# Optimization experiments

Measured on AMD Instinct MI355X. Metric: run time of the kernel, lower is better.

The kernel has to match this reference:

```python
import math
import jax, jax.numpy as jnp
import numpy as np

B, L, S, H, E, D = 2, 2048, 2048, 8, 64, 64


def setup_inputs() -> dict:
    key = jax.random.key(0)
    kq, kk, kv = jax.random.split(key, 3)
    return {
        "queries": jax.random.normal(kq, (B, L, H, E), dtype=jnp.float32),
        "keys": jax.random.normal(kk, (B, S, H, E), dtype=jnp.float32),
        "values": jax.random.normal(kv, (B, S, H, D), dtype=jnp.float32),
    }


def reference(queries, keys, values):
    b, l, h, e = queries.shape
    s = keys.shape[1]
    # source truncates queries if L > S
    if l > s:
        queries = queries[:, :s]
        l = s
    # dense scores [B,H,L,S]
    scores = jnp.einsum('blhe,bshe->bhls', queries, keys)
    # sparsity measure per query: max - mean over keys
    M_sp = scores.max(axis=-1) - scores.sum(axis=-1) / s  # [B,H,L]
    # k = min(max(L*log(S),1), L); for S>=3 this equals L (all queries, reordered)
    k = min(int(max(l * math.log(s), 1)), l)
    _, top_k = jax.lax.top_k(M_sp, k)  # [B,H,k], descending by M_sp
    # gather selected query rows of the score matrix
    topk_scores = jnp.take_along_axis(scores, top_k[..., None], axis=2)  # [B,H,k,S]
    topk_scores = topk_scores - topk_scores.max(axis=-1, keepdims=True)
    A = jax.nn.softmax(topk_scores / math.sqrt(e), axis=-1)  # [B,H,k,S]
    # attend (output in top-k-permuted query order, as in source)
    V = jnp.einsum('bhls,bshd->blhd', A, values)  # [B,k,H,D]
    return V
```

## Files before the change

kernel.cpp:

```cpp
#include <hip/hip_runtime.h>
#include <math.h>

#define BB 2
#define LL 2048
#define SS 2048
#define HH 8
#define EE 64
#define DD 64
#define HE (HH * EE)


typedef __attribute__((ext_vector_type(8))) short   bf16x8;
typedef __attribute__((ext_vector_type(4))) float   f32x4;
typedef __attribute__((ext_vector_type(8))) unsigned short u16x8;
typedef __attribute__((ext_vector_type(4))) unsigned short u16x4;

__device__ __forceinline__ unsigned short f2bf(float x) {
    unsigned int u = __float_as_uint(x);
    return (unsigned short)((u + 0x7FFFu + ((u >> 16) & 1u)) >> 16);
}

__device__ __forceinline__ float rdlane(float v, int lane) {
    return __uint_as_float(
        (unsigned)__builtin_amdgcn_readlane((int)__float_as_uint(v), lane));
}

__global__ __launch_bounds__(256, 2)
void msp_blas(const float* __restrict__ Q, const float* __restrict__ K,
              float* __restrict__ m32, float* __restrict__ maxs) {
#pragma clang fp contract(off)
    const int bid = blockIdx.x;
    const int lt = bid & 31, bh = bid >> 5;
    const int h = bh & 7, b = bh >> 3;
    const int t = threadIdx.x, lq = t & 63, w = t >> 6;
    const int l = lt * 64 + lq;

    float qf[64];
    const float4* qrow = (const float4*)(Q + (((size_t)b * LL + l) * HH + h) * EE);
#pragma unroll
    for (int i = 0; i < 16; i++) {
        float4 v = qrow[i];
        qf[4*i] = v.x; qf[4*i+1] = v.y; qf[4*i+2] = v.z; qf[4*i+3] = v.w;
    }

    const float* Kw = K + (((size_t)b * SS) * HH + h) * EE + (size_t)w * 512 * HE;
    const float* gld = Kw + (size_t)(lq >> 4) * HE + (lq & 15) * 4;

    float4 A0 = *(const float4*)(gld);
    float4 B0 = *(const float4*)(gld + 4 * HE);

    float mx = -1e30f;
    float blk[4];
#pragma unroll 1
    for (int lf = 0; lf < 4; ++lf) {
        float r[8];
#pragma unroll 1
        for (int i8 = 0; i8 < 16; ++i8) {
            const int kc = lf * 128 + i8 * 8;
            const int kn = (kc < 504) ? kc + 8 : 504;

            float4 A1 = *(const float4*)(gld + (size_t)kn * HE);
            float4 B1 = *(const float4*)(gld + (size_t)(kn + 4) * HE);

            float c[8];
#pragma unroll
            for (int j = 0; j < 8; ++j) c[j] = 0.f;
#pragma unroll
            for (int j = 0; j < 4; ++j) {
#pragma unroll
                for (int e4 = 0; e4 < 16; ++e4) {
                    const int ln = j * 16 + e4;
                    c[j] = fmaf(qf[4*e4+0], rdlane(A0.x, ln), c[j]);
                    c[j] = fmaf(qf[4*e4+1], rdlane(A0.y, ln), c[j]);
                    c[j] = fmaf(qf[4*e4+2], rdlane(A0.z, ln), c[j]);
                    c[j] = fmaf(qf[4*e4+3], rdlane(A0.w, ln), c[j]);
                }
            }
#pragma unroll
            for (int j = 0; j < 4; ++j) {
#pragma unroll
                for (int e4 = 0; e4 < 16; ++e4) {
                    const int ln = j * 16 + e4;
                    c[4+j] = fmaf(qf[4*e4+0], rdlane(B0.x, ln), c[4+j]);
                    c[4+j] = fmaf(qf[4*e4+1], rdlane(B0.y, ln), c[4+j]);
                    c[4+j] = fmaf(qf[4*e4+2], rdlane(B0.z, ln), c[4+j]);
                    c[4+j] = fmaf(qf[4*e4+3], rdlane(B0.w, ln), c[4+j]);
                }
            }
#pragma unroll
            for (int j = 0; j < 8; ++j) {
                mx = fmaxf(mx, c[j]);
                if (i8 == 0) r[j] = c[j];
                else         r[j] = __fadd_rn(r[j], c[j]);
            }
            A0 = A1; B0 = B1;
        }
        blk[lf] = __fadd_rn(
            __fadd_rn(__fadd_rn(r[0], r[1]), __fadd_rn(r[2], r[3])),
            __fadd_rn(__fadd_rn(r[4], r[5]), __fadd_rn(r[6], r[7])));
    }
    const float sub = __fadd_rn(__fadd_rn(blk[0], blk[1]),
                                __fadd_rn(blk[2], blk[3]));

    __shared__ float smx[4][64], ssub[4][64];
    smx[w][lq] = mx; ssub[w][lq] = sub;
    __syncthreads();
    if (w == 0) {
        const float m_all = fmaxf(fmaxf(smx[0][lq], smx[1][lq]),
                                  fmaxf(smx[2][lq], smx[3][lq]));
        const float s2048 = __fadd_rn(__fadd_rn(ssub[0][lq], ssub[1][lq]),
                                      __fadd_rn(ssub[2][lq], ssub[3][lq]));
        const float mean = __fmul_rn(s2048, 0.00048828125f);
        m32[((size_t)bh << 11) + l]  = __fsub_rn(m_all, mean);
        maxs[((size_t)bh << 11) + l] = m_all;
    }
}

__global__ __launch_bounds__(256)
void sort_rank(const float* __restrict__ m32, int* __restrict__ rank) {
    __shared__ unsigned int k1[2048];
    __shared__ int pay[2048];
    const int bh = blockIdx.x;
    const int t = threadIdx.x;
    for (int i = t; i < 2048; i += 256) {
        unsigned int u = __float_as_uint(m32[((size_t)bh << 11) + i]);
        u = (u & 0x80000000u) ? ~u : (u | 0x80000000u);
        k1[i] = u; pay[i] = i;
    }
    __syncthreads();
    for (int k = 2; k <= 2048; k <<= 1) {
        for (int j = k >> 1; j > 0; j >>= 1) {
            for (int i = t; i < 2048; i += 256) {
                const int ixj = i ^ j;
                if (ixj > i) {
                    unsigned int a1 = k1[i], c1 = k1[ixj];
                    int pa = pay[i], pc = pay[ixj];
                    const bool pre = (a1 > c1) || (a1 == c1 && pa < pc);
                    const bool dir = ((i & k) == 0);
                    if (dir != pre) {
                        k1[i] = c1; k1[ixj] = a1;
                        pay[i] = pc; pay[ixj] = pa;
                    }
                }
            }
            __syncthreads();
        }
    }
    for (int i = t; i < 2048; i += 256)
        rank[((size_t)bh << 11) + pay[i]] = i;
}

__global__ __launch_bounds__(256, 2)
void flash_mfma(const float* __restrict__ Q, const float* __restrict__ K,
                const float* __restrict__ V, const float* __restrict__ maxs,
                const int* __restrict__ rank, float* __restrict__ out) {
    __shared__ unsigned short ldsK[2][64 * 72];
    __shared__ unsigned short ldsVT[2][64 * 72];
    __shared__ unsigned short ldsP[4 * 16 * 72];

    const int bid = blockIdx.x;
    const int bh = bid & 15, lt = bid >> 4;
    const int h = bh & 7, b = bh >> 3;
    const int t = threadIdx.x, lane = t & 63, w = t >> 6;
    const int quad = lane >> 4, cl = lane & 15;

    const size_t kvbase = (((size_t)b * SS) * HH + h) * EE;

    bf16x8 qa[2];
    {
        const float* qp = Q + (((size_t)b * LL + (lt * 64 + w * 16 + cl)) * HH + h) * EE
                          + quad * 8;
#pragma unroll
        for (int ef = 0; ef < 2; ++ef) {
            float4 a0 = *(const float4*)(qp + ef * 32);
            float4 a1 = *(const float4*)(qp + ef * 32 + 4);
            short* s = (short*)&qa[ef];
            s[0] = (short)f2bf(a0.x); s[1] = (short)f2bf(a0.y);
            s[2] = (short)f2bf(a0.z); s[3] = (short)f2bf(a0.w);
            s[4] = (short)f2bf(a1.x); s[5] = (short)f2bf(a1.y);
            s[6] = (short)f2bf(a1.z); s[7] = (short)f2bf(a1.w);
        }
    }

    float negpm[4];
    int rk[4];
#pragma unroll
    for (int reg = 0; reg < 4; ++reg) {
        const int qg = lt * 64 + w * 16 + quad * 4 + reg;
        negpm[reg] = -0.125f * maxs[((size_t)bh << 11) + qg];
        rk[reg]    = rank[((size_t)bh << 11) + qg];
    }

    f32x4 accO[4];
#pragma unroll
    for (int nt = 0; nt < 4; ++nt) accO[nt] = (f32x4){0.f, 0.f, 0.f, 0.f};
    float ell[4] = {0.f, 0.f, 0.f, 0.f};

    const int pbase = w * (16 * 72);

    const int krow = t >> 2, kcol = (t & 3) * 16;
    const int vs0 = (t & 15) * 4, vd0 = (t >> 4) * 4;

    {
        const float* gp = K + kvbase + (size_t)krow * HE + kcol;
        float4 f0 = ((const float4*)gp)[0];
        float4 f1 = ((const float4*)gp)[1];
        float4 f2 = ((const float4*)gp)[2];
        float4 f3 = ((const float4*)gp)[3];
        const float* gv = V + kvbase + (size_t)vs0 * HE + vd0;
        float4 v0 = *(const float4*)(gv);
        float4 v1 = *(const float4*)(gv + HE);
        float4 v2 = *(const float4*)(gv + 2 * HE);
        float4 v3 = *(const float4*)(gv + 3 * HE);
        u16x8 w0 = { f2bf(f0.x), f2bf(f0.y), f2bf(f0.z), f2bf(f0.w),
                     f2bf(f1.x), f2bf(f1.y), f2bf(f1.z), f2bf(f1.w) };
        u16x8 w1 = { f2bf(f2.x), f2bf(f2.y), f2bf(f2.z), f2bf(f2.w),
                     f2bf(f3.x), f2bf(f3.y), f2bf(f3.z), f2bf(f3.w) };
        *(u16x8*)&ldsK[0][krow * 72 + kcol]     = w0;
        *(u16x8*)&ldsK[0][krow * 72 + kcol + 8] = w1;
        u16x4 p0 = { f2bf(v0.x), f2bf(v1.x), f2bf(v2.x), f2bf(v3.x) };
        u16x4 p1 = { f2bf(v0.y), f2bf(v1.y), f2bf(v2.y), f2bf(v3.y) };
        u16x4 p2 = { f2bf(v0.z), f2bf(v1.z), f2bf(v2.z), f2bf(v3.z) };
        u16x4 p3 = { f2bf(v0.w), f2bf(v1.w), f2bf(v2.w), f2bf(v3.w) };
        *(u16x4*)&ldsVT[0][(vd0 + 0) * 72 + vs0] = p0;
        *(u16x4*)&ldsVT[0][(vd0 + 1) * 72 + vs0] = p1;
        *(u16x4*)&ldsVT[0][(vd0 + 2) * 72 + vs0] = p2;
        *(u16x4*)&ldsVT[0][(vd0 + 3) * 72 + vs0] = p3;
    }
    __syncthreads();

    int cur = 0;
#pragma unroll 1
    for (int c0 = 0; c0 < SS; c0 += 64) {
        const bool more = (c0 + 64 < SS);
        float4 f0, f1, f2, f3, v0, v1, v2, v3;
        if (more) {
            const float* gp = K + kvbase + (size_t)(c0 + 64 + krow) * HE + kcol;
            f0 = ((const float4*)gp)[0];
            f1 = ((const float4*)gp)[1];
            f2 = ((const float4*)gp)[2];
            f3 = ((const float4*)gp)[3];
            const float* gv = V + kvbase + (size_t)(c0 + 64 + vs0) * HE + vd0;
            v0 = *(const float4*)(gv);
            v1 = *(const float4*)(gv + HE);
            v2 = *(const float4*)(gv + 2 * HE);
            v3 = *(const float4*)(gv + 3 * HE);
        }

        f32x4 Sc[4];
#pragma unroll
        for (int nt = 0; nt < 4; ++nt) {
            bf16x8 bk0 = *(const bf16x8*)&ldsK[cur][(nt * 16 + cl) * 72 + quad * 8];
            bf16x8 bk1 = *(const bf16x8*)&ldsK[cur][(nt * 16 + cl) * 72 + quad * 8 + 32];
            f32x4 z = (f32x4){0.f, 0.f, 0.f, 0.f};
            z = __builtin_amdgcn_mfma_f32_16x16x32_bf16(qa[0], bk0, z, 0, 0, 0);
            z = __builtin_amdgcn_mfma_f32_16x16x32_bf16(qa[1], bk1, z, 0, 0, 0);
            Sc[nt] = z;
        }

#pragma unroll
        for (int nt = 0; nt < 4; ++nt) {
#pragma unroll
            for (int reg = 0; reg < 4; ++reg) {
                const float p = __expf(fmaf(Sc[nt][reg], 0.125f, negpm[reg]));
                ell[reg] += p;
                ldsP[pbase + (quad * 4 + reg) * 72 + nt * 16 + cl] = f2bf(p);
            }
        }

        bf16x8 pa0 = *(const bf16x8*)&ldsP[pbase + cl * 72 + quad * 8];
        bf16x8 pa1 = *(const bf16x8*)&ldsP[pbase + cl * 72 + quad * 8 + 32];
#pragma unroll
        for (int nt = 0; nt < 4; ++nt) {
            bf16x8 bv0 = *(const bf16x8*)&ldsVT[cur][(nt * 16 + cl) * 72 + quad * 8];
            bf16x8 bv1 = *(const bf16x8*)&ldsVT[cur][(nt * 16 + cl) * 72 + quad * 8 + 32];
            accO[nt] = __builtin_amdgcn_mfma_f32_16x16x32_bf16(pa0, bv0, accO[nt], 0, 0, 0);
            accO[nt] = __builtin_amdgcn_mfma_f32_16x16x32_bf16(pa1, bv1, accO[nt], 0, 0, 0);
        }

        if (more) {
            u16x8 w0 = { f2bf(f0.x), f2bf(f0.y), f2bf(f0.z), f2bf(f0.w),
                         f2bf(f1.x), f2bf(f1.y), f2bf(f1.z), f2bf(f1.w) };
            u16x8 w1 = { f2bf(f2.x), f2bf(f2.y), f2bf(f2.z), f2bf(f2.w),
                         f2bf(f3.x), f2bf(f3.y), f2bf(f3.z), f2bf(f3.w) };
            *(u16x8*)&ldsK[cur ^ 1][krow * 72 + kcol]     = w0;
            *(u16x8*)&ldsK[cur ^ 1][krow * 72 + kcol + 8] = w1;
            u16x4 p0 = { f2bf(v0.x), f2bf(v1.x), f2bf(v2.x), f2bf(v3.x) };
            u16x4 p1 = { f2bf(v0.y), f2bf(v1.y), f2bf(v2.y), f2bf(v3.y) };
            u16x4 p2 = { f2bf(v0.z), f2bf(v1.z), f2bf(v2.z), f2bf(v3.z) };
            u16x4 p3 = { f2bf(v0.w), f2bf(v1.w), f2bf(v2.w), f2bf(v3.w) };
            *(u16x4*)&ldsVT[cur ^ 1][(vd0 + 0) * 72 + vs0] = p0;
            *(u16x4*)&ldsVT[cur ^ 1][(vd0 + 1) * 72 + vs0] = p1;
            *(u16x4*)&ldsVT[cur ^ 1][(vd0 + 2) * 72 + vs0] = p2;
            *(u16x4*)&ldsVT[cur ^ 1][(vd0 + 3) * 72 + vs0] = p3;
        }
        __syncthreads();
        cur ^= 1;
    }

#pragma unroll
    for (int reg = 0; reg < 4; ++reg) {
        float e = ell[reg];
        e += __shfl_xor(e, 1);
        e += __shfl_xor(e, 2);
        e += __shfl_xor(e, 4);
        e += __shfl_xor(e, 8);
        ell[reg] = 1.0f / e;
    }

#pragma unroll
    for (int reg = 0; reg < 4; ++reg) {
        float* orow = out + (((size_t)b * LL + rk[reg]) * HH + h) * DD;
#pragma unroll
        for (int nt = 0; nt < 4; ++nt)
            orow[nt * 16 + cl] = accO[nt][reg] * ell[reg];
    }
}

extern "C" void kernel_launch(void* const* d_in, const int* in_sizes, int n_in,
                              void* d_out, int out_size, void* d_ws, size_t ws_size,
                              hipStream_t stream) {
    const float* Q = (const float*)d_in[0];
    const float* K = (const float*)d_in[1];
    const float* V = (const float*)d_in[2];
    float* out = (float*)d_out;

    float* m32  = (float*)d_ws;
    int*   rank = (int*)((char*)d_ws + 131072);
    float* maxs = (float*)((char*)d_ws + 262144);

    msp_blas<<<BB * HH * (LL / 64), 256, 0, stream>>>(Q, K, m32, maxs);
    sort_rank<<<BB * HH, 256, 0, stream>>>(m32, rank);
    flash_mfma<<<BB * HH * (LL / 64), 256, 0, stream>>>(Q, K, V, maxs, rank, out);
}
```

Measured before the change: 401.3 us.

## Split sparsity-measure kernel over two key halves and merge partials in sort kernel

The score max/sum kernel now launches twice as many blocks, each covering half of the keys, and writes partial max and sum values to scratch. The output buffer is reused as that scratch. The sort kernel combines the partials into the final max and mean before sorting. The aim is to fill more compute units in the first stage (512 blocks was a small grid for a CU-heavy GPU), at the cost of an extra scratch round-trip and slightly more work in the single-block-per-head sort kernel.

Measured after the change: 389.6 us. 1.03x faster.

```diff
diff --git a/kernel.cpp b/kernel.cpp
--- a/kernel.cpp
+++ b/kernel.cpp
@@ -26,11 +26,13 @@
 }
 
 __global__ __launch_bounds__(256, 2)
-void msp_blas(const float* __restrict__ Q, const float* __restrict__ K,
-              float* __restrict__ m32, float* __restrict__ maxs) {
+void msp_partial(const float* __restrict__ Q, const float* __restrict__ K,
+                 float* __restrict__ pscratch) {
 #pragma clang fp contract(off)
     const int bid = blockIdx.x;
-    const int lt = bid & 31, bh = bid >> 5;
+    const int hf = bid >> 9;
+    const int rem = bid & 511;
+    const int lt = rem & 31, bh = rem >> 5;
     const int h = bh & 7, b = bh >> 3;
     const int t = threadIdx.x, lq = t & 63, w = t >> 6;
     const int l = lt * 64 + lq;
@@ -43,21 +45,22 @@
         qf[4*i] = v.x; qf[4*i+1] = v.y; qf[4*i+2] = v.z; qf[4*i+3] = v.w;
     }
 
-    const float* Kw = K + (((size_t)b * SS) * HH + h) * EE + (size_t)w * 512 * HE;
+    const float* Kw = K + (((size_t)b * SS) * HH + h) * EE
+                        + (size_t)(hf * 1024 + w * 256) * HE;
     const float* gld = Kw + (size_t)(lq >> 4) * HE + (lq & 15) * 4;
 
     float4 A0 = *(const float4*)(gld);
     float4 B0 = *(const float4*)(gld + 4 * HE);
 
     float mx = -1e30f;
-    float blk[4];
+    float blkv[2];
 #pragma unroll 1
-    for (int lf = 0; lf < 4; ++lf) {
+    for (int lb = 0; lb < 2; ++lb) {
         float r[8];
 #pragma unroll 1
         for (int i8 = 0; i8 < 16; ++i8) {
-            const int kc = lf * 128 + i8 * 8;
-            const int kn = (kc < 504) ? kc + 8 : 504;
+            const int kc = lb * 128 + i8 * 8;
+            const int kn = (kc < 248) ? kc + 8 : 248;
 
             float4 A1 = *(const float4*)(gld + (size_t)kn * HE);
             float4 B1 = *(const float4*)(gld + (size_t)(kn + 4) * HE);
@@ -95,35 +98,50 @@
             }
             A0 = A1; B0 = B1;
         }
-        blk[lf] = __fadd_rn(
+        blkv[lb] = __fadd_rn(
             __fadd_rn(__fadd_rn(r[0], r[1]), __fadd_rn(r[2], r[3])),
             __fadd_rn(__fadd_rn(r[4], r[5]), __fadd_rn(r[6], r[7])));
     }
-    const float sub = __fadd_rn(__fadd_rn(blk[0], blk[1]),
-                                __fadd_rn(blk[2], blk[3]));
-
-    __shared__ float smx[4][64], ssub[4][64];
-    smx[w][lq] = mx; ssub[w][lq] = sub;
+
+    __shared__ float smx[4][64];
+    __shared__ float sblk[8][64];
+    smx[w][lq] = mx;
+    sblk[2 * w + 0][lq] = blkv[0];
+    sblk[2 * w + 1][lq] = blkv[1];
     __syncthreads();
     if (w == 0) {
         const float m_all = fmaxf(fmaxf(smx[0][lq], smx[1][lq]),
                                   fmaxf(smx[2][lq], smx[3][lq]));
-        const float s2048 = __fadd_rn(__fadd_rn(ssub[0][lq], ssub[1][lq]),
-                                      __fadd_rn(ssub[2][lq], ssub[3][lq]));
-        const float mean = __fmul_rn(s2048, 0.00048828125f);
-        m32[((size_t)bh << 11) + l]  = __fsub_rn(m_all, mean);
-        maxs[((size_t)bh << 11) + l] = m_all;
+        const float sub_lo = __fadd_rn(
+            __fadd_rn(sblk[0][lq], sblk[1][lq]),
+            __fadd_rn(sblk[2][lq], sblk[3][lq]));
+        const float sub_hi = __fadd_rn(
+            __fadd_rn(sblk[4][lq], sblk[5][lq]),
+            __fadd_rn(sblk[6][lq], sblk[7][lq]));
+        const float psum = __fadd_rn(sub_lo, sub_hi);
+        pscratch[(((size_t)hf * 16 + bh) << 11) + l]         = m_all;
+        pscratch[65536 + (((size_t)hf * 16 + bh) << 11) + l] = psum;
     }
 }
 
 __global__ __launch_bounds__(256)
-void sort_rank(const float* __restrict__ m32, int* __restrict__ rank) {
+void sort_rank(const float* __restrict__ pscratch, float* __restrict__ maxs,
+               int* __restrict__ rank) {
     __shared__ unsigned int k1[2048];
     __shared__ int pay[2048];
     const int bh = blockIdx.x;
     const int t = threadIdx.x;
     for (int i = t; i < 2048; i += 256) {
-        unsigned int u = __float_as_uint(m32[((size_t)bh << 11) + i]);
+        const float pmax0 = pscratch[(((size_t)bh) << 11) + i];
+        const float pmax1 = pscratch[(((size_t)16 + bh) << 11) + i];
+        const float psum0 = pscratch[65536 + (((size_t)bh) << 11) + i];
+        const float psum1 = pscratch[65536 + (((size_t)16 + bh) << 11) + i];
+        const float m_all = fmaxf(pmax0, pmax1);
+        const float s2048 = __fadd_rn(psum0, psum1);
+        const float mean  = __fmul_rn(s2048, 0.00048828125f);
+        const float msp   = __fsub_rn(m_all, mean);
+        maxs[(((size_t)bh) << 11) + i] = m_all;
+        unsigned int u = __float_as_uint(msp);
         u = (u & 0x80000000u) ? ~u : (u | 0x80000000u);
         k1[i] = u; pay[i] = i;
     }
@@ -147,7 +165,7 @@
         }
     }
     for (int i = t; i < 2048; i += 256)
-        rank[((size_t)bh << 11) + pay[i]] = i;
+        rank[(((size_t)bh) << 11) + pay[i]] = i;
 }
 
 __global__ __launch_bounds__(256, 2)
@@ -325,11 +343,10 @@
     const float* V = (const float*)d_in[2];
     float* out = (float*)d_out;
 
-    float* m32  = (float*)d_ws;
     int*   rank = (int*)((char*)d_ws + 131072);
     float* maxs = (float*)((char*)d_ws + 262144);
 
-    msp_blas<<<BB * HH * (LL / 64), 256, 0, stream>>>(Q, K, m32, maxs);
-    sort_rank<<<BB * HH, 256, 0, stream>>>(m32, rank);
+    msp_partial<<<2 * BB * HH * (LL / 64), 256, 0, stream>>>(Q, K, out);
+    sort_rank<<<BB * HH, 256, 0, stream>>>(out, maxs, rank);
     flash_mfma<<<BB * HH * (LL / 64), 256, 0, stream>>>(Q, K, V, maxs, rank, out);
 }
```
